# Optimization experiments

Hardware: AMD Instinct MI355X
Metric: run time of the kernel (lower is better)

## Reference

```python
import math
import jax, jax.numpy as jnp
import numpy as np

D_MODEL = 1024
N_HEADS = 16
HEAD_DIM = D_MODEL // N_HEADS
FEATURE_DIM = 16
WINDOW = 64
EPS_NORM = 1e-6
EPS_DEN = 1e-6

_TRIU_I, _TRIU_J = np.triu_indices(FEATURE_DIM)

def taylor_feature_map(x):
    # x: [B,T,H,f] -> [B,T,H,1+f+f(f+1)/2]
    B, T, H, d = x.shape
    ones = jnp.ones((B, T, H, 1), dtype=x.dtype)
    outer = jnp.einsum('bthd,bthe->bthde', x, x)
    scale = jnp.full((d, d), 1.0 / math.sqrt(2), dtype=x.dtype)
    scale = scale.at[jnp.arange(d), jnp.arange(d)].set(0.5)
    outer = outer * scale
    quadratic = outer[..., _TRIU_I, _TRIU_J]
    return jnp.concatenate([ones, x, quadratic], axis=-1)

def rmsnorm(x, w):
    var = jnp.mean(x * x, axis=-1, keepdims=True)
    return x * jax.lax.rsqrt(var + EPS_NORM) * w

def setup_inputs() -> dict:
    key = jax.random.key(0)
    ks = jax.random.split(key, 9)
    B, T = 2, 2048
    std = 0.02
    return {
        'x': jax.random.normal(ks[0], (B, T, D_MODEL), jnp.float32),
        'encoder_out': jax.random.normal(ks[1], (B, T, D_MODEL), jnp.float32),
        'norm_w': jnp.ones((D_MODEL,), jnp.float32),
        'Wq': jax.random.normal(ks[2], (D_MODEL, D_MODEL), jnp.float32) * std,
        'Wkv': jax.random.normal(ks[3], (D_MODEL, 2 * D_MODEL), jnp.float32) * std,
        'Wqf': jax.random.normal(ks[4], (HEAD_DIM, FEATURE_DIM), jnp.float32) * std,
        'Wkf': jax.random.normal(ks[5], (HEAD_DIM, FEATURE_DIM), jnp.float32) * std,
        'Wwin': jax.random.normal(ks[6], (D_MODEL, 2 * D_MODEL), jnp.float32) * std,
        'Wout': jax.random.normal(ks[7], (2 * D_MODEL, D_MODEL), jnp.float32) * std,
    }

def _forward(x, encoder_out, norm_w, Wq, Wkv, Wqf, Wkf, Wwin, Wout):
    residual = x
    xn = rmsnorm(x, norm_w)
    B, T_dec, _ = xn.shape
    T_enc = encoder_out.shape[1]
    H, hd = N_HEADS, HEAD_DIM

    q = (xn @ Wq).reshape(B, T_dec, H, hd)
    kv = (encoder_out @ Wkv).reshape(B, T_enc, 2, H, hd)
    k, v = kv[:, :, 0], kv[:, :, 1]

    # Taylor linear cross-attention
    q_phi = taylor_feature_map(q @ Wqf)   # [B,T_dec,H,F]
    k_phi = taylor_feature_map(k @ Wkf)   # [B,T_enc,H,F]
    kv_state = jnp.einsum('bshf,bshd->bhfd', k_phi, v)
    k_state = k_phi.sum(axis=1)           # [B,H,F]
    linear_out = jnp.einsum('bthf,bhfd->bthd', q_phi, kv_state)
    normalizer = jnp.einsum('bthf,bhf->bth', q_phi, k_state)[..., None]
    linear_out = (linear_out / (normalizer + EPS_DEN)).reshape(B, T_dec, D_MODEL)

    # Sliding-window causal self-attention (flash window_size=(WINDOW,0))
    kv_win = (xn @ Wwin).reshape(B, T_dec, 2, H, hd)
    k_win, v_win = kv_win[:, :, 0], kv_win[:, :, 1]
    scores = jnp.einsum('bthd,bshd->bhts', q, k_win) * (1.0 / math.sqrt(hd))
    i = jnp.arange(T_dec)[:, None]
    j = jnp.arange(T_dec)[None, :]
    allowed = (j <= i) & (j >= i - WINDOW)
    scores = jnp.where(allowed, scores, jnp.finfo(scores.dtype).min)
    probs = jax.nn.softmax(scores, axis=-1)
    window_out = jnp.einsum('bhts,bshd->bthd', probs, v_win).reshape(B, T_dec, D_MODEL)

    combined = jnp.concatenate([linear_out, window_out], axis=-1)
    return residual + combined @ Wout

def reference(x, encoder_out, norm_w, Wq, Wkv, Wqf, Wkf, Wwin, Wout):
    return _forward(x, encoder_out, norm_w, Wq, Wkv, Wqf, Wkf, Wwin, Wout)
```

## Files before the change

kernel.cpp:

```cpp
#include <hip/hip_runtime.h>

#define DM 1024
#define NH 16
#define HD 64
#define FD 16
#define NF 153
#define FPAD 160
#define WIN 64
#define TSEQ 2048
#define ROWS 4096
#define KSPLIT 8
#define RS2 0.70710678118654752f

typedef unsigned short u16;
typedef __attribute__((ext_vector_type(8))) short bf16x8;
typedef __attribute__((ext_vector_type(8))) unsigned short u16x8;
typedef __attribute__((ext_vector_type(4))) unsigned short u16x4;
typedef __attribute__((ext_vector_type(4))) float f32x4;

#define GLB_AS __attribute__((address_space(1)))
#define LDS_AS __attribute__((address_space(3)))

static __device__ __forceinline__ void gload_lds16(const void* g, void* l){
  __builtin_amdgcn_global_load_lds((const GLB_AS void*)g, (LDS_AS void*)l, 16, 0, 0);
}

static __device__ __forceinline__ float bf2f(u16 u){
  unsigned v = ((unsigned)u) << 16;
  return __builtin_bit_cast(float, v);
}
static __device__ __forceinline__ u16 f2bf(float f){
  unsigned u = __builtin_bit_cast(unsigned, f);
  u += 0x7FFFu + ((u >> 16) & 1u);
  return (u16)(u >> 16);
}

__global__ __launch_bounds__(256) void k_prep(const float* __restrict__ x,
    const float* __restrict__ enc, const float* __restrict__ w,
    u16* __restrict__ xn, u16* __restrict__ encb){
  int row = blockIdx.x, tid = threadIdx.x;
  if (blockIdx.y == 0){
    const float4* xr = (const float4*)(x + (size_t)row*DM);
    float4 a = xr[tid];
    float ss = a.x*a.x + a.y*a.y + a.z*a.z + a.w*a.w;
    #pragma unroll
    for (int m=1;m<64;m<<=1) ss += __shfl_xor(ss, m);
    __shared__ float red[4];
    if ((tid&63)==0) red[tid>>6] = ss;
    __syncthreads();
    float tot = red[0]+red[1]+red[2]+red[3];
    float rs = rsqrtf(tot*(1.0f/DM) + 1e-6f);
    float4 wv = ((const float4*)w)[tid];
    u16x4 o;
    o[0]=f2bf(a.x*rs*wv.x); o[1]=f2bf(a.y*rs*wv.y);
    o[2]=f2bf(a.z*rs*wv.z); o[3]=f2bf(a.w*rs*wv.w);
    ((u16x4*)(xn + (size_t)row*DM))[tid] = o;
  } else {
    float4 a = ((const float4*)(enc + (size_t)row*DM))[tid];
    u16x4 o;
    o[0]=f2bf(a.x); o[1]=f2bf(a.y); o[2]=f2bf(a.z); o[3]=f2bf(a.w);
    ((u16x4*)(encb + (size_t)row*DM))[tid] = o;
  }
}

static __device__ __forceinline__ void tr_tile(const float* __restrict__ in,
    u16* __restrict__ out, int K, int N, int n0, int k0, float* t, int tid){
  int tx = tid & 31, ty = tid >> 5;
  #pragma unroll
  for (int i=0;i<4;i++) t[(ty + i*8)*33 + tx] = in[(size_t)(k0 + ty + i*8)*N + n0 + tx];
  __syncthreads();
  #pragma unroll
  for (int i=0;i<4;i++) out[(size_t)(n0 + ty + i*8)*K + k0 + tx] = f2bf(t[tx*33 + ty + i*8]);
}

__global__ __launch_bounds__(256) void k_packw(const float* __restrict__ Wq,
    const float* __restrict__ Wwin, const float* __restrict__ Wkv,
    const float* __restrict__ Wout, const float* __restrict__ Wqf,
    const float* __restrict__ Wkf, u16* __restrict__ WqwT, u16* __restrict__ WkvT,
    u16* __restrict__ WoutT, u16* __restrict__ WqfT, u16* __restrict__ WkfT){
  __shared__ float t[32*33];
  int b = blockIdx.x, tid = threadIdx.x;
  if (b < 1024){
    tr_tile(Wq, WqwT, 1024, 1024, (b&31)*32, (b>>5)*32, t, tid);
  } else if (b < 3072){
    int r = b-1024;
    tr_tile(Wwin, WqwT + (size_t)1024*1024, 1024, 2048, (r&63)*32, (r>>6)*32, t, tid);
  } else if (b < 5120){
    int r = b-3072;
    tr_tile(Wkv, WkvT, 1024, 2048, (r&63)*32, (r>>6)*32, t, tid);
  } else if (b < 7168){
    int r = b-5120;
    tr_tile(Wout, WoutT, 2048, 1024, (r&31)*32, (r>>5)*32, t, tid);
  } else {
    const float* src = (b==7168) ? Wqf : Wkf;
    u16* dst = (b==7168) ? WqfT : WkfT;
    for (int i=tid;i<1024;i+=256) dst[i] = f2bf(src[(i&63)*16 + (i>>6)]);
  }
}

template<int EPI>
__global__ __launch_bounds__(256) void k_gemm(
    const u16* __restrict__ A0, const u16* __restrict__ B0, u16* __restrict__ C0, int ldc0,
    const u16* __restrict__ A1, const u16* __restrict__ B1, u16* __restrict__ C1, int ldc1,
    int split, int K, float* __restrict__ Cf, const float* __restrict__ resid){
  __shared__ u16 As0[128*64];
  __shared__ u16 Bs0[128*64];
  __shared__ u16 As1[128*64];
  __shared__ u16 Bs1[128*64];
  int by = blockIdx.y;
  const u16 *A, *Bt; u16* C; int ldc;
  if (by < split){ A=A0; Bt=B0; C=C0; ldc=ldc0; }
  else { by -= split; A=A1; Bt=B1; C=C1; ldc=ldc1; }
  int row0 = blockIdx.x*128, col0 = by*128;
  int tid = threadIdx.x, lane = tid&63, wid = tid>>6;
  int wr = wid>>1, wc = wid&1;
  int srow = lane>>3;
  int scb  = ((lane&7)*16) ^ (srow<<4);
  f32x4 acc[4][4] = {};

  auto STAGE = [&](u16* Asb, u16* Bsb, int k0){
    #pragma unroll
    for (int i=0;i<4;i++){
      int chunk = wid + i*4;
      int r = chunk*8 + srow;
      gload_lds16((const char*)(A  + (size_t)(row0+r)*K + k0) + scb, (char*)Asb + chunk*1024);
      gload_lds16((const char*)(Bt + (size_t)(col0+r)*K + k0) + scb, (char*)Bsb + chunk*1024);
    }
  };
  auto COMPUTE = [&](const u16* Asb, const u16* Bsb){
    #pragma unroll
    for (int kk=0;kk<64;kk+=32){
      int bc = 2*(kk + ((lane>>4)<<3));
      bf16x8 af[4], bfm[4];
      #pragma unroll
      for (int m=0;m<4;m++){
        int r = wr*64 + m*16 + (lane&15);
        af[m]  = *(const bf16x8*)((const char*)Asb + r*128 + (bc ^ ((r&7)<<4)));
      }
      #pragma unroll
      for (int n=0;n<4;n++){
        int r = wc*64 + n*16 + (lane&15);
        bfm[n] = *(const bf16x8*)((const char*)Bsb + r*128 + (bc ^ ((r&7)<<4)));
      }
      #pragma unroll
      for (int m=0;m<4;m++)
        #pragma unroll
        for (int n=0;n<4;n++)
          acc[m][n] = __builtin_amdgcn_mfma_f32_16x16x32_bf16(af[m], bfm[n], acc[m][n], 0,0,0);
    }
  };

  int nt = K >> 6;
  STAGE(As0, Bs0, 0);
  for (int t=0; t<nt-2; t+=2){
    STAGE(As1, Bs1, (t+1)*64);
    asm volatile("s_waitcnt vmcnt(8)" ::: "memory");
    __builtin_amdgcn_s_barrier();
    COMPUTE(As0, Bs0);
    __builtin_amdgcn_s_barrier();
    STAGE(As0, Bs0, (t+2)*64);
    asm volatile("s_waitcnt vmcnt(8)" ::: "memory");
    __builtin_amdgcn_s_barrier();
    COMPUTE(As1, Bs1);
    __builtin_amdgcn_s_barrier();
  }
  STAGE(As1, Bs1, (nt-1)*64);
  asm volatile("s_waitcnt vmcnt(8)" ::: "memory");
  __builtin_amdgcn_s_barrier();
  COMPUTE(As0, Bs0);
  asm volatile("s_waitcnt vmcnt(0)" ::: "memory");
  __builtin_amdgcn_s_barrier();
  COMPUTE(As1, Bs1);

  int rl = (lane>>4)<<2;
  #pragma unroll
  for (int m=0;m<4;m++){
    #pragma unroll
    for (int n=0;n<4;n++){
      int gc = col0 + wc*64 + n*16 + (lane&15);
      #pragma unroll
      for (int r=0;r<4;r++){
        size_t gi = (size_t)(row0 + wr*64 + m*16 + rl + r)*ldc + gc;
        if constexpr (EPI) Cf[gi] = acc[m][n][r] + resid[gi];
        else               C[gi]  = f2bf(acc[m][n][r]);
      }
    }
  }
}

__global__ __launch_bounds__(256) void k_kvstate(const u16* __restrict__ kvb,
    const u16* __restrict__ WkfT, float* __restrict__ part){
  const int P = 76;
  __shared__ u16 kc[64*64];
  __shared__ u16 wb[16*72];
  __shared__ float fL[64*16];
  __shared__ u16 ph[160*P];
  __shared__ u16 vt[80*P];
  int bh = blockIdx.x, b = bh>>4, h = bh&15;
  int ks = blockIdx.y;
  int tid = threadIdx.x, lane = tid&63, w = tid>>6;
  int srow = lane>>3;
  int scb  = ((lane&7)*16) ^ (srow<<4);
  for (int i=tid;i<1024;i+=256) wb[(i>>6)*72 + (i&63)] = WkfT[i];
  for (int i=tid; i<16*P; i+=256){
    int r = 64 + i/P, c = i - (i/P)*P;
    vt[r*P + c] = (r==64) ? (u16)0x3F80 : (u16)0;
  }
  f32x4 acc[5][3] = {};
  for (int c=0;c<4;c++){
    int s0 = ks*256 + c*64;
    __syncthreads();
    #pragma unroll
    for (int i=0;i<2;i++){
      int ch = w + i*4;
      int r = ch*8 + srow;
      gload_lds16((const char*)(kvb + (size_t)(b*TSEQ + s0 + r)*2048 + h*HD) + scb,
                  (char*)kc + ch*1024);
    }
    for (int s = w; s < 64; s += 4)
      vt[lane*P + s] = kvb[(size_t)(b*TSEQ + s0 + s)*2048 + 1024 + h*HD + lane];
    __syncthreads();
    {
      f32x4 fa = {};
      #pragma unroll
      for (int kk=0;kk<2;kk++){
        int bc = 2*(kk*32 + ((lane>>4)<<3));
        int r = w*16 + (lane&15);
        bf16x8 av = *(const bf16x8*)((const char*)kc + r*128 + (bc ^ ((r&7)<<4)));
        bf16x8 bv = *(const bf16x8*)(wb + (lane&15)*72 + kk*32 + ((lane>>4)<<3));
        fa = __builtin_amdgcn_mfma_f32_16x16x32_bf16(av, bv, fa, 0,0,0);
      }
      int rl = (lane>>4)<<2;
      #pragma unroll
      for (int r=0;r<4;r++) fL[(w*16 + rl + r)*16 + (lane&15)] = fa[r];
    }
    __syncthreads();
    {
      int r = tid>>2, jq = tid&3;
      float4 v0 = *(const float4*)(fL + r*16 + 0);
      float4 v1 = *(const float4*)(fL + r*16 + 4);
      float4 v2 = *(const float4*)(fL + r*16 + 8);
      float4 v3 = *(const float4*)(fL + r*16 + 12);
      float f[16] = {v0.x,v0.y,v0.z,v0.w, v1.x,v1.y,v1.z,v1.w,
                     v2.x,v2.y,v2.z,v2.w, v3.x,v3.y,v3.z,v3.w};
      if ((0&3)==jq) ph[0*P + r] = 0x3F80;
      #pragma unroll
      for (int q=0;q<16;q++) if (((1+q)&3)==jq) ph[(1+q)*P + r] = f2bf(f[q]);
      int pos = 17;
      #pragma unroll
      for (int i=0;i<16;i++)
        #pragma unroll
        for (int j=i;j<16;j++){
          if ((pos&3)==jq) ph[pos*P + r] = f2bf(f[i]*f[j]*((i==j)?0.5f:RS2));
          pos++;
        }
      #pragma unroll
      for (int z=153;z<160;z++) if ((z&3)==jq) ph[z*P + r] = 0;
    }
    __syncthreads();
    #pragma unroll
    for (int kk=0;kk<2;kk++){
      int lk = kk*32 + ((lane>>4)<<3);
      bf16x8 bfr[3];
      #pragma unroll
      for (int nn=0;nn<3;nn++){
        int ncol = (nn<2) ? (w*2+nn) : (8+(w&1));
        bfr[nn] = *(const bf16x8*)(ph + (ncol*16 + (lane&15))*P + lk);
      }
      #pragma unroll
      for (int m=0;m<5;m++){
        bf16x8 av = *(const bf16x8*)(vt + (m*16 + (lane&15))*P + lk);
        #pragma unroll
        for (int nn=0;nn<3;nn++)
          acc[m][nn] = __builtin_amdgcn_mfma_f32_16x16x32_bf16(av, bfr[nn], acc[m][nn], 0,0,0);
      }
    }
  }
  int rl = (lane>>4)<<2;
  float* pp = part + ((size_t)ks*32 + bh)*80*160;
  #pragma unroll
  for (int m=0;m<5;m++){
    #pragma unroll
    for (int nn=0;nn<3;nn++){
      int ncol = (nn<2) ? (w*2+nn) : (8+(w&1));
      if (nn==2 && w>=2) continue;
      int fcol = ncol*16 + (lane&15);
      #pragma unroll
      for (int r=0;r<4;r++)
        pp[(size_t)(m*16 + rl + r)*160 + fcol] = acc[m][nn][r];
    }
  }
}

__global__ __launch_bounds__(256) void k_kvreduce(const float* __restrict__ part,
    u16* __restrict__ kvsT){
  int i = blockIdx.x*256 + threadIdx.x;
  float s = 0.f;
  #pragma unroll
  for (int c=0;c<KSPLIT;c++) s += part[(size_t)c*409600 + i];
  kvsT[i] = f2bf(s);
}

__global__ __launch_bounds__(256) void k_linattn(const u16* __restrict__ qwin,
    const u16* __restrict__ WqfT, const u16* __restrict__ kvsT, u16* __restrict__ comb){
  const int LS = 168;
  __shared__ u16 As[64*LS];
  __shared__ u16 Bs[80*LS];
  __shared__ u16 qc[64*64];
  __shared__ u16 wb[16*72];
  __shared__ float fL[64*16];
  int bh = blockIdx.x, b = bh>>4, h = bh&15;
  int t0 = blockIdx.y*64;
  int tid = threadIdx.x, lane = tid&63, wid = tid>>6;
  int srow = lane>>3;
  int scb  = ((lane&7)*16) ^ (srow<<4);
  for (int i=tid;i<1024;i+=256) wb[(i>>6)*72 + (i&63)] = WqfT[i];
  for (int i=tid*8; i<80*FPAD; i+=2048){
    int r = i/FPAD, ff = i - r*FPAD;
    *(bf16x8*)(Bs + r*LS + ff) = *(const bf16x8*)(kvsT + (size_t)bh*80*FPAD + i);
  }
  #pragma unroll
  for (int i=0;i<2;i++){
    int ch = wid + i*4;
    int r = ch*8 + srow;
    gload_lds16((const char*)(qwin + (size_t)(b*TSEQ + t0 + r)*3072 + h*HD) + scb,
                (char*)qc + ch*1024);
  }
  __syncthreads();
  {
    f32x4 fa = {};
    #pragma unroll
    for (int kk=0;kk<2;kk++){
      int bc = 2*(kk*32 + ((lane>>4)<<3));
      int r = wid*16 + (lane&15);
      bf16x8 av = *(const bf16x8*)((const char*)qc + r*128 + (bc ^ ((r&7)<<4)));
      bf16x8 bv = *(const bf16x8*)(wb + (lane&15)*72 + kk*32 + ((lane>>4)<<3));
      fa = __builtin_amdgcn_mfma_f32_16x16x32_bf16(av, bv, fa, 0,0,0);
    }
    int rl = (lane>>4)<<2;
    #pragma unroll
    for (int r=0;r<4;r++) fL[(wid*16 + rl + r)*16 + (lane&15)] = fa[r];
  }
  __syncthreads();
  {
    int r = tid>>2, jq = tid&3;
    float4 v0 = *(const float4*)(fL + r*16 + 0);
    float4 v1 = *(const float4*)(fL + r*16 + 4);
    float4 v2 = *(const float4*)(fL + r*16 + 8);
    float4 v3 = *(const float4*)(fL + r*16 + 12);
    float f[16] = {v0.x,v0.y,v0.z,v0.w, v1.x,v1.y,v1.z,v1.w,
                   v2.x,v2.y,v2.z,v2.w, v3.x,v3.y,v3.z,v3.w};
    if ((0&3)==jq) As[r*LS + 0] = 0x3F80;
    #pragma unroll
    for (int q=0;q<16;q++) if (((1+q)&3)==jq) As[r*LS + 1+q] = f2bf(f[q]);
    int pos = 17;
    #pragma unroll
    for (int i=0;i<16;i++)
      #pragma unroll
      for (int j=i;j<16;j++){
        if ((pos&3)==jq) As[r*LS + pos] = f2bf(f[i]*f[j]*((i==j)?0.5f:RS2));
        pos++;
      }
    #pragma unroll
    for (int z=153;z<160;z++) if ((z&3)==jq) As[r*LS + z] = 0;
  }
  __syncthreads();
  f32x4 acc[5] = {};
  #pragma unroll
  for (int ks=0;ks<5;ks++){
    int lk = ks*32 + ((lane>>4)<<3);
    bf16x8 a = *(const bf16x8*)(As + (wid*16 + (lane&15))*LS + lk);
    #pragma unroll
    for (int n=0;n<5;n++){
      bf16x8 bb = *(const bf16x8*)(Bs + (n*16 + (lane&15))*LS + lk);
      acc[n] = __builtin_amdgcn_mfma_f32_16x16x32_bf16(a, bb, acc[n], 0,0,0);
    }
  }
  int rl = (lane>>4)<<2;
  #pragma unroll
  for (int r=0;r<4;r++){
    float nrm = __shfl(acc[4][r], lane & 48) + 1e-6f;
    float inv = 1.0f / nrm;
    int t = t0 + wid*16 + rl + r;
    #pragma unroll
    for (int n=0;n<4;n++){
      comb[(size_t)(b*TSEQ + t)*2048 + h*64 + n*16 + (lane&15)] = f2bf(acc[n][r]*inv);
    }
  }
}

__global__ __launch_bounds__(256) void k_window(const u16* __restrict__ q, int ldq,
    const u16* __restrict__ kvwin, int ldkv, u16* __restrict__ comb){
  const int LQ = 72, LV = 136;
  __shared__ u16 q_s [64*LQ];
  __shared__ u16 k_s [128*LQ];
  __shared__ u16 vT_s[64*LV];
  __shared__ u16 p_s [64*LV];
  int bh = blockIdx.x, b = bh>>4, h = bh&15;
  int t0 = blockIdx.y*64;
  int tid = threadIdx.x, lane = tid&63, wid = tid>>6;
  int j0 = t0 - 64;
  bf16x8 zv = {0,0,0,0,0,0,0,0};
  for (int cc=tid; cc<512; cc+=256){
    int r = cc>>3, c8 = cc&7;
    *(bf16x8*)(q_s + r*LQ + c8*8) =
      *(const bf16x8*)(q + (size_t)(b*TSEQ + t0 + r)*ldq + h*HD + c8*8);
  }
  for (int cc=tid; cc<1024; cc+=256){
    int r = cc>>3, c8 = cc&7;
    int j = j0 + r;
    bf16x8 kv8 = (j>=0) ? *(const bf16x8*)(kvwin + (size_t)(b*TSEQ + j)*ldkv + h*HD + c8*8) : zv;
    *(bf16x8*)(k_s + r*LQ + c8*8) = kv8;
    bf16x8 vv8 = (j>=0) ? *(const bf16x8*)(kvwin + (size_t)(b*TSEQ + j)*ldkv + 1024 + h*HD + c8*8) : zv;
    #pragma unroll
    for (int e=0;e<8;e++) vT_s[(c8*8+e)*LV + r] = (u16)vv8[e];
  }
  __syncthreads();
  f32x4 sa[8] = {};
  #pragma unroll
  for (int kk=0;kk<64;kk+=32){
    int lk = kk + ((lane>>4)<<3);
    bf16x8 a = *(const bf16x8*)(q_s + (wid*16 + (lane&15))*LQ + lk);
    #pragma unroll
    for (int n=0;n<8;n++){
      bf16x8 bb = *(const bf16x8*)(k_s + (n*16 + (lane&15))*LQ + lk);
      sa[n] = __builtin_amdgcn_mfma_f32_16x16x32_bf16(a, bb, sa[n], 0,0,0);
    }
  }
  int rl = (lane>>4)<<2;
  float pr[8][4];
  #pragma unroll
  for (int r=0;r<4;r++){
    int ig = t0 + wid*16 + rl + r;
    float mx = -1e30f;
    float sv[8];
    #pragma unroll
    for (int n=0;n<8;n++){
      int jg = j0 + n*16 + (lane&15);
      float s = sa[n][r]*0.125f;
      bool ok = (jg>=0) && (jg<=ig) && (jg>=ig-WIN);
      s = ok ? s : -1e30f;
      sv[n]=s; mx = fmaxf(mx, s);
    }
    #pragma unroll
    for (int m=1;m<16;m<<=1) mx = fmaxf(mx, __shfl_xor(mx, m));
    float sum = 0.f;
    #pragma unroll
    for (int n=0;n<8;n++){ float e = __expf(sv[n]-mx); sv[n]=e; sum += e; }
    #pragma unroll
    for (int m=1;m<16;m<<=1) sum += __shfl_xor(sum, m);
    float inv = 1.0f/sum;
    #pragma unroll
    for (int n=0;n<8;n++) pr[n][r] = sv[n]*inv;
  }
  #pragma unroll
  for (int n=0;n<8;n++)
    #pragma unroll
    for (int r=0;r<4;r++)
      p_s[(wid*16 + rl + r)*LV + n*16 + (lane&15)] = f2bf(pr[n][r]);
  __syncthreads();
  f32x4 oa[4] = {};
  #pragma unroll
  for (int ks=0;ks<4;ks++){
    int lk = ks*32 + ((lane>>4)<<3);
    bf16x8 a = *(const bf16x8*)(p_s + (wid*16 + (lane&15))*LV + lk);
    #pragma unroll
    for (int n=0;n<4;n++){
      bf16x8 bb = *(const bf16x8*)(vT_s + (n*16 + (lane&15))*LV + lk);
      oa[n] = __builtin_amdgcn_mfma_f32_16x16x32_bf16(a, bb, oa[n], 0,0,0);
    }
  }
  #pragma unroll
  for (int n=0;n<4;n++)
    #pragma unroll
    for (int r=0;r<4;r++)
      comb[(size_t)(b*TSEQ + t0 + wid*16 + rl + r)*2048 + 1024 + h*HD + n*16 + (lane&15)]
        = f2bf(oa[n][r]);
}

extern "C" void kernel_launch(void* const* d_in, const int* in_sizes, int n_in,
                              void* d_out, int out_size, void* d_ws, size_t ws_size,
                              hipStream_t stream){
  (void)in_sizes; (void)n_in; (void)out_size; (void)ws_size;
  const float* x    = (const float*)d_in[0];
  const float* enc  = (const float*)d_in[1];
  const float* nw   = (const float*)d_in[2];
  const float* Wq   = (const float*)d_in[3];
  const float* Wkv  = (const float*)d_in[4];
  const float* Wqf  = (const float*)d_in[5];
  const float* Wkf  = (const float*)d_in[6];
  const float* Wwin = (const float*)d_in[7];
  const float* Wout = (const float*)d_in[8];
  float* out = (float*)d_out;

  char* p = (char*)d_ws;
  auto alloc = [&](size_t bytes)->char*{
    char* r = p; p += (bytes + 255) & ~(size_t)255; return r;
  };
  char*  aliasBase = p;
  u16*   xn    = (u16*)  alloc((size_t)ROWS*DM*2);
  u16*   encb  = (u16*)  alloc((size_t)ROWS*DM*2);
  u16*   WqwT  = (u16*)  alloc((size_t)3072*DM*2);
  u16*   WkvT  = (u16*)  alloc((size_t)2048*DM*2);
  float* part  = (float*)aliasBase;
  u16*   WoutT = (u16*)  alloc((size_t)DM*2048*2);
  u16*   WqfT  = (u16*)  alloc((size_t)FD*HD*2);
  u16*   WkfT  = (u16*)  alloc((size_t)FD*HD*2);
  u16*   qwin  = (u16*)  alloc((size_t)ROWS*3072*2);
  u16*   kvb   = (u16*)  alloc((size_t)ROWS*2048*2);
  u16*   kvsT  = (u16*)  alloc((size_t)32*80*FPAD*2);
  u16*   comb  = (u16*)  alloc((size_t)ROWS*2048*2);

  k_prep <<<dim3(ROWS, 2), 256, 0, stream>>>(x, enc, nw, xn, encb);
  k_packw<<<7170, 256, 0, stream>>>(Wq, Wwin, Wkv, Wout, Wqf, Wkf,
                                    WqwT, WkvT, WoutT, WqfT, WkfT);

  k_gemm<0><<<dim3(ROWS/128, 40), 256, 0, stream>>>(
      xn, WqwT, qwin, 3072,  encb, WkvT, kvb, 2048,  24, DM, nullptr, nullptr);

  k_kvstate<<<dim3(32, KSPLIT), 256, 0, stream>>>(kvb, WkfT, part);
  k_kvreduce<<<1600, 256, 0, stream>>>(part, kvsT);

  k_linattn<<<dim3(32, TSEQ/64), 256, 0, stream>>>(qwin, WqfT, kvsT, comb);
  k_window <<<dim3(32, TSEQ/64), 256, 0, stream>>>(qwin, 3072, qwin + 1024, 3072, comb);

  k_gemm<1><<<dim3(ROWS/128, 8), 256, 0, stream>>>(
      comb, WoutT, nullptr, DM,  nullptr, nullptr, nullptr, 0,  8, 2048, out, x);
}
```

Measured before the change: 171.2 us.

## Use 8-wave GEMM blocks and merge weight packing into prep kernel

The GEMM kernel now runs 512 threads (8 waves) per 128x128 tile, with each wave owning a 64x32 sub-tile instead of 64x64. This halves per-wave accumulators and staging loads and raises the number of waves available to hide latency, at the cost of more LDS fragment reloads of A per MFMA. Separately, the weight transpose/pack kernel is folded into the prep kernel as extra blocks, removing one launch and letting both jobs run concurrently.

```diff
diff --git a/kernel.cpp b/kernel.cpp
--- a/kernel.cpp
+++ b/kernel.cpp
@@ -35,11 +35,28 @@
   return (u16)(u >> 16);
 }
 
+static __device__ __forceinline__ void tr_tile(const float* __restrict__ in,
+    u16* __restrict__ out, int K, int N, int n0, int k0, float* t, int tid){
+  int tx = tid & 31, ty = tid >> 5;
+  #pragma unroll
+  for (int i=0;i<4;i++) t[(ty + i*8)*33 + tx] = in[(size_t)(k0 + ty + i*8)*N + n0 + tx];
+  __syncthreads();
+  #pragma unroll
+  for (int i=0;i<4;i++) out[(size_t)(n0 + ty + i*8)*K + k0 + tx] = f2bf(t[tx*33 + ty + i*8]);
+}
+
 __global__ __launch_bounds__(256) void k_prep(const float* __restrict__ x,
     const float* __restrict__ enc, const float* __restrict__ w,
-    u16* __restrict__ xn, u16* __restrict__ encb){
-  int row = blockIdx.x, tid = threadIdx.x;
-  if (blockIdx.y == 0){
+    const float* __restrict__ Wq, const float* __restrict__ Wwin,
+    const float* __restrict__ Wkv, const float* __restrict__ Wout,
+    const float* __restrict__ Wqf, const float* __restrict__ Wkf,
+    u16* __restrict__ xn, u16* __restrict__ encb,
+    u16* __restrict__ WqwT, u16* __restrict__ WkvT, u16* __restrict__ WoutT,
+    u16* __restrict__ WqfT, u16* __restrict__ WkfT){
+  __shared__ float t[32*33];
+  int bx = blockIdx.x, tid = threadIdx.x;
+  if (bx < ROWS){
+    int row = bx;
     const float4* xr = (const float4*)(x + (size_t)row*DM);
     float4 a = xr[tid];
     float ss = a.x*a.x + a.y*a.y + a.z*a.z + a.w*a.w;
@@ -55,51 +72,35 @@
     o[0]=f2bf(a.x*rs*wv.x); o[1]=f2bf(a.y*rs*wv.y);
     o[2]=f2bf(a.z*rs*wv.z); o[3]=f2bf(a.w*rs*wv.w);
     ((u16x4*)(xn + (size_t)row*DM))[tid] = o;
-  } else {
+  } else if (bx < 2*ROWS){
+    int row = bx - ROWS;
     float4 a = ((const float4*)(enc + (size_t)row*DM))[tid];
     u16x4 o;
     o[0]=f2bf(a.x); o[1]=f2bf(a.y); o[2]=f2bf(a.z); o[3]=f2bf(a.w);
     ((u16x4*)(encb + (size_t)row*DM))[tid] = o;
-  }
-}
-
-static __device__ __forceinline__ void tr_tile(const float* __restrict__ in,
-    u16* __restrict__ out, int K, int N, int n0, int k0, float* t, int tid){
-  int tx = tid & 31, ty = tid >> 5;
-  #pragma unroll
-  for (int i=0;i<4;i++) t[(ty + i*8)*33 + tx] = in[(size_t)(k0 + ty + i*8)*N + n0 + tx];
-  __syncthreads();
-  #pragma unroll
-  for (int i=0;i<4;i++) out[(size_t)(n0 + ty + i*8)*K + k0 + tx] = f2bf(t[tx*33 + ty + i*8]);
-}
-
-__global__ __launch_bounds__(256) void k_packw(const float* __restrict__ Wq,
-    const float* __restrict__ Wwin, const float* __restrict__ Wkv,
-    const float* __restrict__ Wout, const float* __restrict__ Wqf,
-    const float* __restrict__ Wkf, u16* __restrict__ WqwT, u16* __restrict__ WkvT,
-    u16* __restrict__ WoutT, u16* __restrict__ WqfT, u16* __restrict__ WkfT){
-  __shared__ float t[32*33];
-  int b = blockIdx.x, tid = threadIdx.x;
-  if (b < 1024){
-    tr_tile(Wq, WqwT, 1024, 1024, (b&31)*32, (b>>5)*32, t, tid);
-  } else if (b < 3072){
-    int r = b-1024;
-    tr_tile(Wwin, WqwT + (size_t)1024*1024, 1024, 2048, (r&63)*32, (r>>6)*32, t, tid);
-  } else if (b < 5120){
-    int r = b-3072;
-    tr_tile(Wkv, WkvT, 1024, 2048, (r&63)*32, (r>>6)*32, t, tid);
-  } else if (b < 7168){
-    int r = b-5120;
-    tr_tile(Wout, WoutT, 2048, 1024, (r&31)*32, (r>>5)*32, t, tid);
   } else {
-    const float* src = (b==7168) ? Wqf : Wkf;
-    u16* dst = (b==7168) ? WqfT : WkfT;
-    for (int i=tid;i<1024;i+=256) dst[i] = f2bf(src[(i&63)*16 + (i>>6)]);
+    int b = bx - 2*ROWS;
+    if (b < 1024){
+      tr_tile(Wq, WqwT, 1024, 1024, (b&31)*32, (b>>5)*32, t, tid);
+    } else if (b < 3072){
+      int r = b-1024;
+      tr_tile(Wwin, WqwT + (size_t)1024*1024, 1024, 2048, (r&63)*32, (r>>6)*32, t, tid);
+    } else if (b < 5120){
+      int r = b-3072;
+      tr_tile(Wkv, WkvT, 1024, 2048, (r&63)*32, (r>>6)*32, t, tid);
+    } else if (b < 7168){
+      int r = b-5120;
+      tr_tile(Wout, WoutT, 2048, 1024, (r&31)*32, (r>>5)*32, t, tid);
+    } else {
+      const float* src = (b==7168) ? Wqf : Wkf;
+      u16* dst = (b==7168) ? WqfT : WkfT;
+      for (int i=tid;i<1024;i+=256) dst[i] = f2bf(src[(i&63)*16 + (i>>6)]);
+    }
   }
 }
 
 template<int EPI>
-__global__ __launch_bounds__(256) void k_gemm(
+__global__ __launch_bounds__(512) void k_gemm(
     const u16* __restrict__ A0, const u16* __restrict__ B0, u16* __restrict__ C0, int ldc0,
     const u16* __restrict__ A1, const u16* __restrict__ B1, u16* __restrict__ C1, int ldc1,
     int split, int K, float* __restrict__ Cf, const float* __restrict__ resid){
@@ -113,15 +114,15 @@
   else { by -= split; A=A1; Bt=B1; C=C1; ldc=ldc1; }
   int row0 = blockIdx.x*128, col0 = by*128;
   int tid = threadIdx.x, lane = tid&63, wid = tid>>6;
-  int wr = wid>>1, wc = wid&1;
+  int wm = wid>>2, wn = wid&3;
   int srow = lane>>3;
   int scb  = ((lane&7)*16) ^ (srow<<4);
-  f32x4 acc[4][4] = {};
+  f32x4 acc[4][2] = {};
 
   auto STAGE = [&](u16* Asb, u16* Bsb, int k0){
     #pragma unroll
-    for (int i=0;i<4;i++){
-      int chunk = wid + i*4;
+    for (int i=0;i<2;i++){
+      int chunk = wid*2 + i;
       int r = chunk*8 + srow;
       gload_lds16((const char*)(A  + (size_t)(row0+r)*K + k0) + scb, (char*)Asb + chunk*1024);
       gload_lds16((const char*)(Bt + (size_t)(col0+r)*K + k0) + scb, (char*)Bsb + chunk*1024);
@@ -131,21 +132,21 @@
     #pragma unroll
     for (int kk=0;kk<64;kk+=32){
       int bc = 2*(kk + ((lane>>4)<<3));
-      bf16x8 af[4], bfm[4];
+      bf16x8 af[4], bfm[2];
       #pragma unroll
       for (int m=0;m<4;m++){
-        int r = wr*64 + m*16 + (lane&15);
+        int r = wm*64 + m*16 + (lane&15);
         af[m]  = *(const bf16x8*)((const char*)Asb + r*128 + (bc ^ ((r&7)<<4)));
       }
       #pragma unroll
-      for (int n=0;n<4;n++){
-        int r = wc*64 + n*16 + (lane&15);
+      for (int n=0;n<2;n++){
+        int r = wn*32 + n*16 + (lane&15);
         bfm[n] = *(const bf16x8*)((const char*)Bsb + r*128 + (bc ^ ((r&7)<<4)));
       }
       #pragma unroll
       for (int m=0;m<4;m++)
         #pragma unroll
-        for (int n=0;n<4;n++)
+        for (int n=0;n<2;n++)
           acc[m][n] = __builtin_amdgcn_mfma_f32_16x16x32_bf16(af[m], bfm[n], acc[m][n], 0,0,0);
     }
   };
@@ -154,18 +155,18 @@
   STAGE(As0, Bs0, 0);
   for (int t=0; t<nt-2; t+=2){
     STAGE(As1, Bs1, (t+1)*64);
-    asm volatile("s_waitcnt vmcnt(8)" ::: "memory");
+    asm volatile("s_waitcnt vmcnt(4)" ::: "memory");
     __builtin_amdgcn_s_barrier();
     COMPUTE(As0, Bs0);
     __builtin_amdgcn_s_barrier();
     STAGE(As0, Bs0, (t+2)*64);
-    asm volatile("s_waitcnt vmcnt(8)" ::: "memory");
+    asm volatile("s_waitcnt vmcnt(4)" ::: "memory");
     __builtin_amdgcn_s_barrier();
     COMPUTE(As1, Bs1);
     __builtin_amdgcn_s_barrier();
   }
   STAGE(As1, Bs1, (nt-1)*64);
-  asm volatile("s_waitcnt vmcnt(8)" ::: "memory");
+  asm volatile("s_waitcnt vmcnt(4)" ::: "memory");
   __builtin_amdgcn_s_barrier();
   COMPUTE(As0, Bs0);
   asm volatile("s_waitcnt vmcnt(0)" ::: "memory");
@@ -176,11 +177,11 @@
   #pragma unroll
   for (int m=0;m<4;m++){
     #pragma unroll
-    for (int n=0;n<4;n++){
-      int gc = col0 + wc*64 + n*16 + (lane&15);
+    for (int n=0;n<2;n++){
+      int gc = col0 + wn*32 + n*16 + (lane&15);
       #pragma unroll
       for (int r=0;r<4;r++){
-        size_t gi = (size_t)(row0 + wr*64 + m*16 + rl + r)*ldc + gc;
+        size_t gi = (size_t)(row0 + wm*64 + m*16 + rl + r)*ldc + gc;
         if constexpr (EPI) Cf[gi] = acc[m][n][r] + resid[gi];
         else               C[gi]  = f2bf(acc[m][n][r]);
       }
@@ -511,11 +512,10 @@
   u16*   kvsT  = (u16*)  alloc((size_t)32*80*FPAD*2);
   u16*   comb  = (u16*)  alloc((size_t)ROWS*2048*2);
 
-  k_prep <<<dim3(ROWS, 2), 256, 0, stream>>>(x, enc, nw, xn, encb);
-  k_packw<<<7170, 256, 0, stream>>>(Wq, Wwin, Wkv, Wout, Wqf, Wkf,
-                                    WqwT, WkvT, WoutT, WqfT, WkfT);
-
-  k_gemm<0><<<dim3(ROWS/128, 40), 256, 0, stream>>>(
+  k_prep<<<2*ROWS + 7170, 256, 0, stream>>>(x, enc, nw, Wq, Wwin, Wkv, Wout, Wqf, Wkf,
+                                            xn, encb, WqwT, WkvT, WoutT, WqfT, WkfT);
+
+  k_gemm<0><<<dim3(ROWS/128, 40), 512, 0, stream>>>(
       xn, WqwT, qwin, 3072,  encb, WkvT, kvb, 2048,  24, DM, nullptr, nullptr);
 
   k_kvstate<<<dim3(32, KSPLIT), 256, 0, stream>>>(kvb, WkfT, part);
@@ -524,6 +524,6 @@
   k_linattn<<<dim3(32, TSEQ/64), 256, 0, stream>>>(qwin, WqfT, kvsT, comb);
   k_window <<<dim3(32, TSEQ/64), 256, 0, stream>>>(qwin, 3072, qwin + 1024, 3072, comb);
 
-  k_gemm<1><<<dim3(ROWS/128, 8), 256, 0, stream>>>(
+  k_gemm<1><<<dim3(ROWS/128, 8), 512, 0, stream>>>(
       comb, WoutT, nullptr, DM,  nullptr, nullptr, nullptr, 0,  8, 2048, out, x);
 }
```

New measurement: 162.8 us. 1.05x faster.
